# Performance work log

Hardware: AMD Instinct MI355X
Metric: run time of the kernel (lower is better)

Reference implementation:

```python
import jax, jax.numpy as jnp
import numpy as np

DIM = 256
HEADS = 8
WIN = 8
N = WIN * WIN          # 64 tokens per window
NW = 1024              # windows per image (256x256 map, 8x8 windows)
BATCH = 4
B_ = BATCH * NW        # 4096
HEAD_DIM = DIM // HEADS


def _relative_position_index():
    # identical to the torch buffer construction in WindowAttention.__init__
    coords = np.stack(np.meshgrid(np.arange(WIN), np.arange(WIN), indexing='ij'))  # [2,W,W]
    flat = coords.reshape(2, -1)                                # [2, N]
    rel = flat[:, :, None] - flat[:, None, :]                   # [2, N, N]
    rel = rel.transpose(1, 2, 0).copy()                         # [N, N, 2]
    rel[:, :, 0] += WIN - 1
    rel[:, :, 1] += WIN - 1
    rel[:, :, 0] *= 2 * WIN - 1
    return jnp.asarray(rel.sum(-1), dtype=jnp.int32)            # [N, N], values in [0, 225)


def setup_inputs() -> dict:
    key = jax.random.key(0)
    ks = jax.random.split(key, 9)
    std = 0.02
    return {
        'x': jax.random.normal(ks[0], (B_, N, DIM), dtype=jnp.float32),
        'mask': jax.random.normal(ks[1], (NW, N, N), dtype=jnp.float32),
        'w_q': jax.random.normal(ks[2], (DIM, DIM), dtype=jnp.float32) * std,
        'b_q': jnp.zeros((DIM,), dtype=jnp.float32),
        'w_kv': jax.random.normal(ks[3], (2 * DIM, DIM), dtype=jnp.float32) * std,
        'b_kv': jnp.zeros((2 * DIM,), dtype=jnp.float32),
        'bias_table': jax.random.normal(ks[4], ((2 * WIN - 1) ** 2, HEADS), dtype=jnp.float32) * std,
        'w_o': jax.random.normal(ks[5], (DIM, DIM), dtype=jnp.float32) * std,
        'b_o': jnp.zeros((DIM,), dtype=jnp.float32),
        'rp_index': _relative_position_index(),
    }


def reference(x, mask, w_q, b_q, w_kv, b_kv, bias_table, w_o, b_o, rp_index):
    Bw, n, c = x.shape
    h, d = HEADS, c // HEADS
    scale = d ** -0.5

    # linear QKV projection (LinearProjection with attn_kv=None)
    q = (x @ w_q.T + b_q).reshape(Bw, n, h, d).transpose(0, 2, 1, 3)      # [B_, H, N, D]
    kv = (x @ w_kv.T + b_kv).reshape(Bw, n, 2, h, d).transpose(2, 0, 3, 1, 4)
    k, v = kv[0], kv[1]                                                    # [B_, H, N, D]

    # scaled QK^T
    attn = jnp.einsum('bhnd,bhmd->bhnm', q * scale, k)                     # [B_, H, N, N]

    # gathered relative position bias (ratio = 1 since attn_kv is None)
    bias = bias_table[rp_index]                                            # [N, N, H]
    attn = attn + bias.transpose(2, 0, 1)[None]                            # broadcast over B_

    # per-window additive mask
    nW = mask.shape[0]
    attn = attn.reshape(Bw // nW, nW, h, n, n) + mask[None, :, None]
    attn = attn.reshape(Bw, h, n, n)

    attn = jax.nn.softmax(attn, axis=-1)

    out = jnp.einsum('bhnm,bhmd->bhnd', attn, v)                           # [B_, H, N, D]
    out = out.transpose(0, 2, 1, 3).reshape(Bw, n, c)
    return out @ w_o.T + b_o
```

## Files before the change

### kernel.cpp

```cpp
#include <hip/hip_runtime.h>
#include <hip/hip_bf16.h>

typedef __bf16 bf16_t;
typedef bf16_t bf16x8 __attribute__((ext_vector_type(8)));
typedef bf16_t bf16x4 __attribute__((ext_vector_type(4)));
typedef float f32x4 __attribute__((ext_vector_type(4)));

#define WS_WKV_OFF 65536
#define WS_WO_OFF  196608
#define WS_B8_OFF  524288

__global__ __launch_bounds__(256) void prep_kernel(
    const float* __restrict__ wq, const float* __restrict__ wkv,
    const float* __restrict__ wo, const float* __restrict__ bt,
    const int* __restrict__ rp,
    bf16_t* __restrict__ wsq, bf16_t* __restrict__ wskv,
    bf16_t* __restrict__ wso, float* __restrict__ bias8) {
  int t = blockIdx.x * 256 + threadIdx.x;
  if (t < 65536)  wsq[t]  = (bf16_t)wq[t];
  if (t < 131072) wskv[t] = (bf16_t)wkv[t];
  if (t < 65536)  wso[t]  = (bf16_t)wo[t];
  if (t < 4096) {
    int idx = rp[t];
#pragma unroll
    for (int h = 0; h < 8; ++h) bias8[h * 4096 + t] = bt[idx * 8 + h];
  }
}

#define LDS_TOTAL_BYTES 152576

__global__ __launch_bounds__(512, 2) void win_attn_kernel(
    const float* __restrict__ x, const float* __restrict__ mask,
    const float* __restrict__ bq, const float* __restrict__ bkv,
    const float* __restrict__ bo,
    const bf16_t* __restrict__ wsq, const bf16_t* __restrict__ wskv,
    const bf16_t* __restrict__ wso, const float* __restrict__ bias8,
    float* __restrict__ out) {
  extern __shared__ bf16_t lds[];
  const int b    = blockIdx.x;
  const int tid  = threadIdx.x;
  const int wid  = tid >> 6;
  const int lane = tid & 63;
  const int lrow = lane & 15;
  const int lgrp = lane >> 4;

  {
    const float4* xv = (const float4*)(x + (size_t)b * 16384);
#pragma unroll
    for (int j = 0; j < 8; ++j) {
      int i4 = j * 512 + tid;
      float4 v = xv[i4];
      int e = i4 * 4;
      int r = e >> 8, c = e & 255;
      bf16x4 w = {(bf16_t)v.x, (bf16_t)v.y, (bf16_t)v.z, (bf16_t)v.w};
      *(bf16x4*)(lds + r * 264 + c) = w;
    }
  }
  __syncthreads();

  const int h = wid;
  bf16_t* ldsQ  = lds + 16896 + wid * 7424;
  bf16_t* ldsK  = ldsQ + 2560;
  bf16_t* ldsVt = ldsQ + 5120;
  bf16_t* ldsP  = ldsQ;
  bf16_t* ldsO  = lds;

  const bf16_t* WQh = wsq  + h * 32 * 256;
  const bf16_t* WKh = wskv + h * 32 * 256;
  const bf16_t* WVh = wskv + (256 + h * 32) * 256;
  f32x4 aq[4][2], ak[4][2], av[4][2];
  const f32x4 zf = {0.f, 0.f, 0.f, 0.f};
#pragma unroll
  for (int tm = 0; tm < 4; ++tm)
#pragma unroll
    for (int tn = 0; tn < 2; ++tn) { aq[tm][tn] = zf; ak[tm][tn] = zf; av[tm][tn] = zf; }

#pragma unroll
  for (int ks = 0; ks < 8; ++ks) {
    bf16x8 af[4];
#pragma unroll
    for (int tm = 0; tm < 4; ++tm)
      af[tm] = *(const bf16x8*)(lds + (tm * 16 + lrow) * 264 + ks * 32 + lgrp * 8);
    bf16x8 bqf[2], bkf[2], bvf[2];
#pragma unroll
    for (int tn = 0; tn < 2; ++tn) {
      int wr = (tn * 16 + lrow) * 256 + ks * 32 + lgrp * 8;
      bqf[tn] = *(const bf16x8*)(WQh + wr);
      bkf[tn] = *(const bf16x8*)(WKh + wr);
      bvf[tn] = *(const bf16x8*)(WVh + wr);
    }
#pragma unroll
    for (int tm = 0; tm < 4; ++tm)
#pragma unroll
      for (int tn = 0; tn < 2; ++tn) {
        aq[tm][tn] = __builtin_amdgcn_mfma_f32_16x16x32_bf16(af[tm], bqf[tn], aq[tm][tn], 0, 0, 0);
        ak[tm][tn] = __builtin_amdgcn_mfma_f32_16x16x32_bf16(af[tm], bkf[tn], ak[tm][tn], 0, 0, 0);
        av[tm][tn] = __builtin_amdgcn_mfma_f32_16x16x32_bf16(af[tm], bvf[tn], av[tm][tn], 0, 0, 0);
      }
  }

  const float scale = 0.17677669529663687f;
#pragma unroll
  for (int tn = 0; tn < 2; ++tn) {
    float bqv = bq[h * 32 + tn * 16 + lrow];
    float bkv_ = bkv[h * 32 + tn * 16 + lrow];
    float bvv = bkv[256 + h * 32 + tn * 16 + lrow];
#pragma unroll
    for (int tm = 0; tm < 4; ++tm) {
#pragma unroll
      for (int r = 0; r < 4; ++r) {
        int row = tm * 16 + lgrp * 4 + r;
        ldsQ[row * 40 + tn * 16 + lrow] = (bf16_t)((aq[tm][tn][r] + bqv) * scale);
        ldsK[row * 40 + tn * 16 + lrow] = (bf16_t)(ak[tm][tn][r] + bkv_);
      }
      bf16x4 vv;
#pragma unroll
      for (int r = 0; r < 4; ++r) vv[r] = (bf16_t)(av[tm][tn][r] + bvv);
      *(bf16x4*)(ldsVt + (tn * 16 + lrow) * 72 + tm * 16 + lgrp * 4) = vv;
    }
  }
  __syncthreads();

  f32x4 s[4][4];
  {
    bf16x8 qf[4], kf[4];
#pragma unroll
    for (int t = 0; t < 4; ++t) {
      qf[t] = *(const bf16x8*)(ldsQ + (t * 16 + lrow) * 40 + lgrp * 8);
      kf[t] = *(const bf16x8*)(ldsK + (t * 16 + lrow) * 40 + lgrp * 8);
    }
#pragma unroll
    for (int tm = 0; tm < 4; ++tm)
#pragma unroll
      for (int tc = 0; tc < 4; ++tc)
        s[tm][tc] = __builtin_amdgcn_mfma_f32_16x16x32_bf16(qf[tm], kf[tc], zf, 0, 0, 0);
  }
  const float* maskw = mask + (size_t)(b & 1023) * 4096;
  const float* biash = bias8 + h * 4096;
  float rs[4][4];
#pragma unroll
  for (int tm = 0; tm < 4; ++tm) {
    float val[4][4];
    float mx[4] = {-1e30f, -1e30f, -1e30f, -1e30f};
#pragma unroll
    for (int tc = 0; tc < 4; ++tc)
#pragma unroll
      for (int r = 0; r < 4; ++r) {
        int row = tm * 16 + lgrp * 4 + r, col = tc * 16 + lrow;
        float v = s[tm][tc][r] + biash[row * 64 + col] + maskw[row * 64 + col];
        val[tc][r] = v;
        mx[r] = fmaxf(mx[r], v);
      }
#pragma unroll
    for (int r = 0; r < 4; ++r) {
      float m = mx[r];
      m = fmaxf(m, __shfl_xor(m, 1));
      m = fmaxf(m, __shfl_xor(m, 2));
      m = fmaxf(m, __shfl_xor(m, 4));
      m = fmaxf(m, __shfl_xor(m, 8));
      mx[r] = m;
    }
    float sm[4] = {0.f, 0.f, 0.f, 0.f};
#pragma unroll
    for (int tc = 0; tc < 4; ++tc)
#pragma unroll
      for (int r = 0; r < 4; ++r) {
        float p = __expf(val[tc][r] - mx[r]);
        val[tc][r] = p;
        sm[r] += p;
      }
#pragma unroll
    for (int r = 0; r < 4; ++r) {
      float t = sm[r];
      t += __shfl_xor(t, 1);
      t += __shfl_xor(t, 2);
      t += __shfl_xor(t, 4);
      t += __shfl_xor(t, 8);
      rs[tm][r] = 1.0f / t;
    }
#pragma unroll
    for (int tc = 0; tc < 4; ++tc)
#pragma unroll
      for (int r = 0; r < 4; ++r)
        ldsP[(tm * 16 + lgrp * 4 + r) * 72 + tc * 16 + lrow] = (bf16_t)val[tc][r];
  }

  f32x4 o[4][2];
#pragma unroll
  for (int tm = 0; tm < 4; ++tm)
#pragma unroll
    for (int tn = 0; tn < 2; ++tn) o[tm][tn] = zf;
#pragma unroll
  for (int ks = 0; ks < 2; ++ks) {
    bf16x8 pf[4], vf[2];
#pragma unroll
    for (int tm = 0; tm < 4; ++tm)
      pf[tm] = *(const bf16x8*)(ldsP + (tm * 16 + lrow) * 72 + ks * 32 + lgrp * 8);
#pragma unroll
    for (int tn = 0; tn < 2; ++tn)
      vf[tn] = *(const bf16x8*)(ldsVt + (tn * 16 + lrow) * 72 + ks * 32 + lgrp * 8);
#pragma unroll
    for (int tm = 0; tm < 4; ++tm)
#pragma unroll
      for (int tn = 0; tn < 2; ++tn)
        o[tm][tn] = __builtin_amdgcn_mfma_f32_16x16x32_bf16(pf[tm], vf[tn], o[tm][tn], 0, 0, 0);
  }
#pragma unroll
  for (int tm = 0; tm < 4; ++tm)
#pragma unroll
    for (int tn = 0; tn < 2; ++tn)
#pragma unroll
      for (int r = 0; r < 4; ++r)
        ldsO[(tm * 16 + lgrp * 4 + r) * 264 + h * 32 + tn * 16 + lrow] =
            (bf16_t)(o[tm][tn][r] * rs[tm][r]);
  __syncthreads();

  const int nb = wid * 32;
  f32x4 oc[4][2];
#pragma unroll
  for (int tm = 0; tm < 4; ++tm)
#pragma unroll
    for (int tn = 0; tn < 2; ++tn) oc[tm][tn] = zf;
#pragma unroll
  for (int ks = 0; ks < 8; ++ks) {
    bf16x8 af[4], bf_[2];
#pragma unroll
    for (int tm = 0; tm < 4; ++tm)
      af[tm] = *(const bf16x8*)(ldsO + (tm * 16 + lrow) * 264 + ks * 32 + lgrp * 8);
#pragma unroll
    for (int tn = 0; tn < 2; ++tn)
      bf_[tn] = *(const bf16x8*)(wso + (nb + tn * 16 + lrow) * 256 + ks * 32 + lgrp * 8);
#pragma unroll
    for (int tm = 0; tm < 4; ++tm)
#pragma unroll
      for (int tn = 0; tn < 2; ++tn)
        oc[tm][tn] = __builtin_amdgcn_mfma_f32_16x16x32_bf16(af[tm], bf_[tn], oc[tm][tn], 0, 0, 0);
  }
  float* outw = out + (size_t)b * 16384;
#pragma unroll
  for (int tn = 0; tn < 2; ++tn) {
    float bov = bo[nb + tn * 16 + lrow];
#pragma unroll
    for (int tm = 0; tm < 4; ++tm)
#pragma unroll
      for (int r = 0; r < 4; ++r)
        outw[(tm * 16 + lgrp * 4 + r) * 256 + nb + tn * 16 + lrow] = oc[tm][tn][r] + bov;
  }
}

extern "C" void kernel_launch(void* const* d_in, const int* in_sizes, int n_in,
                              void* d_out, int out_size, void* d_ws, size_t ws_size,
                              hipStream_t stream) {
  const float* x    = (const float*)d_in[0];
  const float* mask = (const float*)d_in[1];
  const float* wq   = (const float*)d_in[2];
  const float* bq   = (const float*)d_in[3];
  const float* wkv  = (const float*)d_in[4];
  const float* bkv  = (const float*)d_in[5];
  const float* bt   = (const float*)d_in[6];
  const float* wo   = (const float*)d_in[7];
  const float* bo   = (const float*)d_in[8];
  const int*   rp   = (const int*)d_in[9];
  float* out = (float*)d_out;

  bf16_t* wsq  = (bf16_t*)d_ws;
  bf16_t* wskv = wsq + WS_WKV_OFF;
  bf16_t* wso  = wsq + WS_WO_OFF;
  float*  bias8 = (float*)((char*)d_ws + WS_B8_OFF);

  prep_kernel<<<512, 256, 0, stream>>>(wq, wkv, wo, bt, rp, wsq, wskv, wso, bias8);

  (void)hipFuncSetAttribute((const void*)win_attn_kernel,
                            hipFuncAttributeMaxDynamicSharedMemorySize, LDS_TOTAL_BYTES);
  win_attn_kernel<<<4096, 512, LDS_TOTAL_BYTES, stream>>>(
      x, mask, bq, bkv, bo, wsq, wskv, wso, bias8, out);
}
```

Measured before the change: 608.1 us.

## Split each window across 16 waves by row slab and stage output through LDS

Block size doubles to 1024 threads. Each head is now handled by two waves, each owning a 32-row slab of the 64 tokens, which halves per-wave MFMA work and register accumulators. The final projection result is staged in LDS and written to global memory with coalesced float4 stores instead of strided scalar stores. This adds extra barriers, and the QKV projection now loads each weight fragment twice per block. The launch bound of 1024 threads with 4 blocks requested may force register pressure or spills, while LDS still limits residency to one block per CU.

```diff
diff --git a/kernel.cpp b/kernel.cpp
--- a/kernel.cpp
+++ b/kernel.cpp
@@ -29,7 +29,7 @@
 
 #define LDS_TOTAL_BYTES 152576
 
-__global__ __launch_bounds__(512, 2) void win_attn_kernel(
+__global__ __launch_bounds__(1024, 4) void win_attn_kernel(
     const float* __restrict__ x, const float* __restrict__ mask,
     const float* __restrict__ bq, const float* __restrict__ bkv,
     const float* __restrict__ bo,
@@ -43,12 +43,15 @@
   const int lane = tid & 63;
   const int lrow = lane & 15;
   const int lgrp = lane >> 4;
+  const int h    = wid & 7;
+  const int slab = wid >> 3;
+  const int r0   = slab * 32;
 
   {
     const float4* xv = (const float4*)(x + (size_t)b * 16384);
 #pragma unroll
-    for (int j = 0; j < 8; ++j) {
-      int i4 = j * 512 + tid;
+    for (int j = 0; j < 4; ++j) {
+      int i4 = j * 1024 + tid;
       float4 v = xv[i4];
       int e = i4 * 4;
       int r = e >> 8, c = e & 255;
@@ -58,29 +61,29 @@
   }
   __syncthreads();
 
-  const int h = wid;
-  bf16_t* ldsQ  = lds + 16896 + wid * 7424;
+  bf16_t* ldsQ  = lds + 16896 + h * 7424;
   bf16_t* ldsK  = ldsQ + 2560;
   bf16_t* ldsVt = ldsQ + 5120;
   bf16_t* ldsP  = ldsQ;
   bf16_t* ldsO  = lds;
+  float*  stage = (float*)(lds + 16896);
 
   const bf16_t* WQh = wsq  + h * 32 * 256;
   const bf16_t* WKh = wskv + h * 32 * 256;
   const bf16_t* WVh = wskv + (256 + h * 32) * 256;
-  f32x4 aq[4][2], ak[4][2], av[4][2];
+  f32x4 aq[2][2], ak[2][2], av[2][2];
   const f32x4 zf = {0.f, 0.f, 0.f, 0.f};
 #pragma unroll
-  for (int tm = 0; tm < 4; ++tm)
+  for (int tm = 0; tm < 2; ++tm)
 #pragma unroll
     for (int tn = 0; tn < 2; ++tn) { aq[tm][tn] = zf; ak[tm][tn] = zf; av[tm][tn] = zf; }
 
 #pragma unroll
   for (int ks = 0; ks < 8; ++ks) {
-    bf16x8 af[4];
-#pragma unroll
-    for (int tm = 0; tm < 4; ++tm)
-      af[tm] = *(const bf16x8*)(lds + (tm * 16 + lrow) * 264 + ks * 32 + lgrp * 8);
+    bf16x8 af[2];
+#pragma unroll
+    for (int tm = 0; tm < 2; ++tm)
+      af[tm] = *(const bf16x8*)(lds + (r0 + tm * 16 + lrow) * 264 + ks * 32 + lgrp * 8);
     bf16x8 bqf[2], bkf[2], bvf[2];
 #pragma unroll
     for (int tn = 0; tn < 2; ++tn) {
@@ -90,7 +93,7 @@
       bvf[tn] = *(const bf16x8*)(WVh + wr);
     }
 #pragma unroll
-    for (int tm = 0; tm < 4; ++tm)
+    for (int tm = 0; tm < 2; ++tm)
 #pragma unroll
       for (int tn = 0; tn < 2; ++tn) {
         aq[tm][tn] = __builtin_amdgcn_mfma_f32_16x16x32_bf16(af[tm], bqf[tn], aq[tm][tn], 0, 0, 0);
@@ -102,51 +105,54 @@
   const float scale = 0.17677669529663687f;
 #pragma unroll
   for (int tn = 0; tn < 2; ++tn) {
-    float bqv = bq[h * 32 + tn * 16 + lrow];
+    float bqv  = bq[h * 32 + tn * 16 + lrow];
     float bkv_ = bkv[h * 32 + tn * 16 + lrow];
-    float bvv = bkv[256 + h * 32 + tn * 16 + lrow];
-#pragma unroll
-    for (int tm = 0; tm < 4; ++tm) {
+    float bvv  = bkv[256 + h * 32 + tn * 16 + lrow];
+#pragma unroll
+    for (int tm = 0; tm < 2; ++tm) {
 #pragma unroll
       for (int r = 0; r < 4; ++r) {
-        int row = tm * 16 + lgrp * 4 + r;
+        int row = r0 + tm * 16 + lgrp * 4 + r;
         ldsQ[row * 40 + tn * 16 + lrow] = (bf16_t)((aq[tm][tn][r] + bqv) * scale);
         ldsK[row * 40 + tn * 16 + lrow] = (bf16_t)(ak[tm][tn][r] + bkv_);
       }
       bf16x4 vv;
 #pragma unroll
       for (int r = 0; r < 4; ++r) vv[r] = (bf16_t)(av[tm][tn][r] + bvv);
-      *(bf16x4*)(ldsVt + (tn * 16 + lrow) * 72 + tm * 16 + lgrp * 4) = vv;
-    }
-  }
-  __syncthreads();
-
-  f32x4 s[4][4];
+      *(bf16x4*)(ldsVt + (tn * 16 + lrow) * 72 + r0 + tm * 16 + lgrp * 4) = vv;
+    }
+  }
+  __syncthreads();
+
+  f32x4 s[2][4];
   {
-    bf16x8 qf[4], kf[4];
-#pragma unroll
-    for (int t = 0; t < 4; ++t) {
-      qf[t] = *(const bf16x8*)(ldsQ + (t * 16 + lrow) * 40 + lgrp * 8);
+    bf16x8 qf[2], kf[4];
+#pragma unroll
+    for (int t = 0; t < 2; ++t)
+      qf[t] = *(const bf16x8*)(ldsQ + (r0 + t * 16 + lrow) * 40 + lgrp * 8);
+#pragma unroll
+    for (int t = 0; t < 4; ++t)
       kf[t] = *(const bf16x8*)(ldsK + (t * 16 + lrow) * 40 + lgrp * 8);
-    }
-#pragma unroll
-    for (int tm = 0; tm < 4; ++tm)
+#pragma unroll
+    for (int tm = 0; tm < 2; ++tm)
 #pragma unroll
       for (int tc = 0; tc < 4; ++tc)
         s[tm][tc] = __builtin_amdgcn_mfma_f32_16x16x32_bf16(qf[tm], kf[tc], zf, 0, 0, 0);
   }
+  __syncthreads();
+
   const float* maskw = mask + (size_t)(b & 1023) * 4096;
   const float* biash = bias8 + h * 4096;
-  float rs[4][4];
-#pragma unroll
-  for (int tm = 0; tm < 4; ++tm) {
+  float rs[2][4];
+#pragma unroll
+  for (int tm = 0; tm < 2; ++tm) {
     float val[4][4];
     float mx[4] = {-1e30f, -1e30f, -1e30f, -1e30f};
 #pragma unroll
     for (int tc = 0; tc < 4; ++tc)
 #pragma unroll
       for (int r = 0; r < 4; ++r) {
-        int row = tm * 16 + lgrp * 4 + r, col = tc * 16 + lrow;
+        int row = r0 + tm * 16 + lgrp * 4 + r, col = tc * 16 + lrow;
         float v = s[tm][tc][r] + biash[row * 64 + col] + maskw[row * 64 + col];
         val[tc][r] = v;
         mx[r] = fmaxf(mx[r], v);
@@ -182,69 +188,81 @@
     for (int tc = 0; tc < 4; ++tc)
 #pragma unroll
       for (int r = 0; r < 4; ++r)
-        ldsP[(tm * 16 + lgrp * 4 + r) * 72 + tc * 16 + lrow] = (bf16_t)val[tc][r];
-  }
-
-  f32x4 o[4][2];
-#pragma unroll
-  for (int tm = 0; tm < 4; ++tm)
+        ldsP[(r0 + tm * 16 + lgrp * 4 + r) * 72 + tc * 16 + lrow] = (bf16_t)val[tc][r];
+  }
+
+  f32x4 o[2][2];
+#pragma unroll
+  for (int tm = 0; tm < 2; ++tm)
 #pragma unroll
     for (int tn = 0; tn < 2; ++tn) o[tm][tn] = zf;
 #pragma unroll
   for (int ks = 0; ks < 2; ++ks) {
-    bf16x8 pf[4], vf[2];
-#pragma unroll
-    for (int tm = 0; tm < 4; ++tm)
-      pf[tm] = *(const bf16x8*)(ldsP + (tm * 16 + lrow) * 72 + ks * 32 + lgrp * 8);
+    bf16x8 pf[2], vf[2];
+#pragma unroll
+    for (int tm = 0; tm < 2; ++tm)
+      pf[tm] = *(const bf16x8*)(ldsP + (r0 + tm * 16 + lrow) * 72 + ks * 32 + lgrp * 8);
 #pragma unroll
     for (int tn = 0; tn < 2; ++tn)
       vf[tn] = *(const bf16x8*)(ldsVt + (tn * 16 + lrow) * 72 + ks * 32 + lgrp * 8);
 #pragma unroll
-    for (int tm = 0; tm < 4; ++tm)
+    for (int tm = 0; tm < 2; ++tm)
 #pragma unroll
       for (int tn = 0; tn < 2; ++tn)
         o[tm][tn] = __builtin_amdgcn_mfma_f32_16x16x32_bf16(pf[tm], vf[tn], o[tm][tn], 0, 0, 0);
   }
 #pragma unroll
-  for (int tm = 0; tm < 4; ++tm)
+  for (int tm = 0; tm < 2; ++tm)
 #pragma unroll
     for (int tn = 0; tn < 2; ++tn)
 #pragma unroll
       for (int r = 0; r < 4; ++r)
-        ldsO[(tm * 16 + lgrp * 4 + r) * 264 + h * 32 + tn * 16 + lrow] =
+        ldsO[(r0 + tm * 16 + lgrp * 4 + r) * 264 + h * 32 + tn * 16 + lrow] =
             (bf16_t)(o[tm][tn][r] * rs[tm][r]);
   __syncthreads();
 
-  const int nb = wid * 32;
-  f32x4 oc[4][2];
-#pragma unroll
-  for (int tm = 0; tm < 4; ++tm)
+  const int nb = h * 32;
+  f32x4 oc[2][2];
+#pragma unroll
+  for (int tm = 0; tm < 2; ++tm)
 #pragma unroll
     for (int tn = 0; tn < 2; ++tn) oc[tm][tn] = zf;
 #pragma unroll
   for (int ks = 0; ks < 8; ++ks) {
-    bf16x8 af[4], bf_[2];
-#pragma unroll
-    for (int tm = 0; tm < 4; ++tm)
-      af[tm] = *(const bf16x8*)(ldsO + (tm * 16 + lrow) * 264 + ks * 32 + lgrp * 8);
+    bf16x8 af[2], bf_[2];
+#pragma unroll
+    for (int tm = 0; tm < 2; ++tm)
+      af[tm] = *(const bf16x8*)(ldsO + (r0 + tm * 16 + lrow) * 264 + ks * 32 + lgrp * 8);
 #pragma unroll
     for (int tn = 0; tn < 2; ++tn)
       bf_[tn] = *(const bf16x8*)(wso + (nb + tn * 16 + lrow) * 256 + ks * 32 + lgrp * 8);
 #pragma unroll
-    for (int tm = 0; tm < 4; ++tm)
+    for (int tm = 0; tm < 2; ++tm)
 #pragma unroll
       for (int tn = 0; tn < 2; ++tn)
         oc[tm][tn] = __builtin_amdgcn_mfma_f32_16x16x32_bf16(af[tm], bf_[tn], oc[tm][tn], 0, 0, 0);
   }
-  float* outw = out + (size_t)b * 16384;
 #pragma unroll
   for (int tn = 0; tn < 2; ++tn) {
     float bov = bo[nb + tn * 16 + lrow];
 #pragma unroll
-    for (int tm = 0; tm < 4; ++tm)
+    for (int tm = 0; tm < 2; ++tm)
 #pragma unroll
       for (int r = 0; r < 4; ++r)
-        outw[(tm * 16 + lgrp * 4 + r) * 256 + nb + tn * 16 + lrow] = oc[tm][tn][r] + bov;
+        stage[(r0 + tm * 16 + lgrp * 4 + r) * 260 + nb + tn * 16 + lrow] =
+            oc[tm][tn][r] + bov;
+  }
+  __syncthreads();
+
+  {
+    float* outw = out + (size_t)b * 16384;
+#pragma unroll
+    for (int j = 0; j < 4; ++j) {
+      int idx = j * 1024 + tid;
+      int r = idx >> 6, c = (idx & 63) * 4;
+      float4 v = *(const float4*)(stage + r * 260 + c);
+      *(float4*)(outw + r * 256 + c) = v;
+    }
   }
 }
 
@@ -272,6 +290,6 @@
 
   (void)hipFuncSetAttribute((const void*)win_attn_kernel,
                             hipFuncAttributeMaxDynamicSharedMemorySize, LDS_TOTAL_BYTES);
-  win_attn_kernel<<<4096, 512, LDS_TOTAL_BYTES, stream>>>(
+  win_attn_kernel<<<4096, 1024, LDS_TOTAL_BYTES, stream>>>(
       x, mask, bq, bkv, bo, wsq, wskv, wso, bias8, out);
 }
```

After: 655.4 us. +7.8%, slower.

## Keep Q/K/V/P in registers via bpermute transposes, shrink LDS for higher occupancy

Applied to the files above, without the earlier changes.

Per-head Q, K, V and softmax probabilities now stay in registers, and MFMA fragments are rearranged with ds_bpermute lane shuffles instead of being staged through per-wave LDS buffers. LDS drops to a single 64x264 bf16 tile, and launch bounds move from 2 to 4 blocks per CU. The Q scale is folded into the bf16 weights in the prep kernel, and scores are computed transposed so mask and bias load as float4. The cost is higher register pressure and extra permute instructions, which may cause spills under the tighter launch bounds.

```diff
diff --git a/kernel.cpp b/kernel.cpp
--- a/kernel.cpp
+++ b/kernel.cpp
@@ -1,14 +1,18 @@
 #include <hip/hip_runtime.h>
 #include <hip/hip_bf16.h>
+#include <stdint.h>
 
 typedef __bf16 bf16_t;
 typedef bf16_t bf16x8 __attribute__((ext_vector_type(8)));
 typedef bf16_t bf16x4 __attribute__((ext_vector_type(4)));
+typedef bf16_t bf16x2 __attribute__((ext_vector_type(2)));
 typedef float f32x4 __attribute__((ext_vector_type(4)));
+typedef uint32_t u32x4 __attribute__((ext_vector_type(4)));
 
 #define WS_WKV_OFF 65536
 #define WS_WO_OFF  196608
 #define WS_B8_OFF  524288
+#define QSCALE 0.17677669529663687f
 
 __global__ __launch_bounds__(256) void prep_kernel(
     const float* __restrict__ wq, const float* __restrict__ wkv,
@@ -17,7 +21,7 @@
     bf16_t* __restrict__ wsq, bf16_t* __restrict__ wskv,
     bf16_t* __restrict__ wso, float* __restrict__ bias8) {
   int t = blockIdx.x * 256 + threadIdx.x;
-  if (t < 65536)  wsq[t]  = (bf16_t)wq[t];
+  if (t < 65536)  wsq[t]  = (bf16_t)(wq[t] * QSCALE);
   if (t < 131072) wskv[t] = (bf16_t)wkv[t];
   if (t < 65536)  wso[t]  = (bf16_t)wo[t];
   if (t < 4096) {
@@ -27,22 +31,48 @@
   }
 }
 
-#define LDS_TOTAL_BYTES 152576
-
-__global__ __launch_bounds__(512, 2) void win_attn_kernel(
+__device__ __forceinline__ bf16x8 xpose_frag(uint32_t e0, uint32_t e1,
+                                             uint32_t o0, uint32_t o1,
+                                             int ad0, int ad1, bool hi) {
+  uint32_t v0e = (uint32_t)__builtin_amdgcn_ds_bpermute(ad0, (int)e0);
+  uint32_t v0o = (uint32_t)__builtin_amdgcn_ds_bpermute(ad0, (int)o0);
+  uint32_t v1e = (uint32_t)__builtin_amdgcn_ds_bpermute(ad0, (int)e1);
+  uint32_t v1o = (uint32_t)__builtin_amdgcn_ds_bpermute(ad0, (int)o1);
+  uint32_t v2e = (uint32_t)__builtin_amdgcn_ds_bpermute(ad1, (int)e0);
+  uint32_t v2o = (uint32_t)__builtin_amdgcn_ds_bpermute(ad1, (int)o0);
+  uint32_t v3e = (uint32_t)__builtin_amdgcn_ds_bpermute(ad1, (int)e1);
+  uint32_t v3o = (uint32_t)__builtin_amdgcn_ds_bpermute(ad1, (int)o1);
+  u32x4 r;
+  r.x = hi ? v0o : v0e;
+  r.y = hi ? v1o : v1e;
+  r.z = hi ? v2o : v2e;
+  r.w = hi ? v3o : v3e;
+  return __builtin_bit_cast(bf16x8, r);
+}
+
+__device__ __forceinline__ uint32_t pk2(float a, float b) {
+  bf16x2 t = {(bf16_t)a, (bf16_t)b};
+  return __builtin_bit_cast(uint32_t, t);
+}
+
+__global__ __launch_bounds__(512, 4) void win_attn_kernel(
     const float* __restrict__ x, const float* __restrict__ mask,
     const float* __restrict__ bq, const float* __restrict__ bkv,
     const float* __restrict__ bo,
     const bf16_t* __restrict__ wsq, const bf16_t* __restrict__ wskv,
     const bf16_t* __restrict__ wso, const float* __restrict__ bias8,
     float* __restrict__ out) {
-  extern __shared__ bf16_t lds[];
+  __shared__ bf16_t lds[64 * 264];
   const int b    = blockIdx.x;
   const int tid  = threadIdx.x;
-  const int wid  = tid >> 6;
+  const int h    = tid >> 6;
   const int lane = tid & 63;
   const int lrow = lane & 15;
   const int lgrp = lane >> 4;
+  const bool hi  = (lgrp & 2) != 0;
+  const int ad0  = ((((2 * lgrp) & 3) << 4) + lrow) << 2;
+  const int ad1  = ((((2 * lgrp + 1) & 3) << 4) + lrow) << 2;
+  const f32x4 zf = {0.f, 0.f, 0.f, 0.f};
 
   {
     const float4* xv = (const float4*)(x + (size_t)b * 16384);
@@ -58,183 +88,190 @@
   }
   __syncthreads();
 
-  const int h = wid;
-  bf16_t* ldsQ  = lds + 16896 + wid * 7424;
-  bf16_t* ldsK  = ldsQ + 2560;
-  bf16_t* ldsVt = ldsQ + 5120;
-  bf16_t* ldsP  = ldsQ;
-  bf16_t* ldsO  = lds;
-
   const bf16_t* WQh = wsq  + h * 32 * 256;
   const bf16_t* WKh = wskv + h * 32 * 256;
-  const bf16_t* WVh = wskv + (256 + h * 32) * 256;
-  f32x4 aq[4][2], ak[4][2], av[4][2];
-  const f32x4 zf = {0.f, 0.f, 0.f, 0.f};
-#pragma unroll
-  for (int tm = 0; tm < 4; ++tm)
-#pragma unroll
-    for (int tn = 0; tn < 2; ++tn) { aq[tm][tn] = zf; ak[tm][tn] = zf; av[tm][tn] = zf; }
-
+  f32x4 aq[2][4], akk[2][4];
+#pragma unroll
+  for (int tm = 0; tm < 2; ++tm)
+#pragma unroll
+    for (int tn = 0; tn < 4; ++tn) { aq[tm][tn] = zf; akk[tm][tn] = zf; }
 #pragma unroll
   for (int ks = 0; ks < 8; ++ks) {
-    bf16x8 af[4];
-#pragma unroll
-    for (int tm = 0; tm < 4; ++tm)
-      af[tm] = *(const bf16x8*)(lds + (tm * 16 + lrow) * 264 + ks * 32 + lgrp * 8);
-    bf16x8 bqf[2], bkf[2], bvf[2];
-#pragma unroll
-    for (int tn = 0; tn < 2; ++tn) {
-      int wr = (tn * 16 + lrow) * 256 + ks * 32 + lgrp * 8;
-      bqf[tn] = *(const bf16x8*)(WQh + wr);
-      bkf[tn] = *(const bf16x8*)(WKh + wr);
-      bvf[tn] = *(const bf16x8*)(WVh + wr);
-    }
+    bf16x8 xb[4];
+#pragma unroll
+    for (int tn = 0; tn < 4; ++tn)
+      xb[tn] = *(const bf16x8*)(lds + (tn * 16 + lrow) * 264 + ks * 32 + lgrp * 8);
+    bf16x8 wqf[2], wkf[2];
+#pragma unroll
+    for (int tm = 0; tm < 2; ++tm) {
+      int off = (tm * 16 + lrow) * 256 + ks * 32 + lgrp * 8;
+      wqf[tm] = *(const bf16x8*)(WQh + off);
+      wkf[tm] = *(const bf16x8*)(WKh + off);
+    }
+#pragma unroll
+    for (int tm = 0; tm < 2; ++tm)
+#pragma unroll
+      for (int tn = 0; tn < 4; ++tn) {
+        aq[tm][tn]  = __builtin_amdgcn_mfma_f32_16x16x32_bf16(wqf[tm], xb[tn], aq[tm][tn], 0, 0, 0);
+        akk[tm][tn] = __builtin_amdgcn_mfma_f32_16x16x32_bf16(wkf[tm], xb[tn], akk[tm][tn], 0, 0, 0);
+      }
+  }
+  bf16x8 qb[4], ka[4];
+  {
+    uint32_t pkq[2][4][2], pkk[2][4][2];
+#pragma unroll
+    for (int tm = 0; tm < 2; ++tm) {
+      float4 b4 = *(const float4*)(bq + h * 32 + tm * 16 + lgrp * 4);
+      float4 k4 = *(const float4*)(bkv + h * 32 + tm * 16 + lgrp * 4);
+      float bqa[4] = {b4.x * QSCALE, b4.y * QSCALE, b4.z * QSCALE, b4.w * QSCALE};
+      float bka[4] = {k4.x, k4.y, k4.z, k4.w};
+#pragma unroll
+      for (int tn = 0; tn < 4; ++tn)
+#pragma unroll
+        for (int pr = 0; pr < 2; ++pr) {
+          pkq[tm][tn][pr] = pk2(aq[tm][tn][2 * pr] + bqa[2 * pr],
+                                aq[tm][tn][2 * pr + 1] + bqa[2 * pr + 1]);
+          pkk[tm][tn][pr] = pk2(akk[tm][tn][2 * pr] + bka[2 * pr],
+                                akk[tm][tn][2 * pr + 1] + bka[2 * pr + 1]);
+        }
+    }
+#pragma unroll
+    for (int t = 0; t < 4; ++t) {
+      qb[t] = xpose_frag(pkq[0][t][0], pkq[0][t][1], pkq[1][t][0], pkq[1][t][1], ad0, ad1, hi);
+      ka[t] = xpose_frag(pkk[0][t][0], pkk[0][t][1], pkk[1][t][0], pkk[1][t][1], ad0, ad1, hi);
+    }
+  }
+
+  bf16x8 vb[2][2];
+  {
+    const bf16_t* WVh = wskv + (256 + h * 32) * 256;
+    f32x4 av[4][2];
+#pragma unroll
+    for (int tm = 0; tm < 4; ++tm)
+#pragma unroll
+      for (int tn = 0; tn < 2; ++tn) av[tm][tn] = zf;
+#pragma unroll
+    for (int ks = 0; ks < 8; ++ks) {
+      bf16x8 xa[4];
+#pragma unroll
+      for (int tm = 0; tm < 4; ++tm)
+        xa[tm] = *(const bf16x8*)(lds + (tm * 16 + lrow) * 264 + ks * 32 + lgrp * 8);
+      bf16x8 wvf[2];
+#pragma unroll
+      for (int tn = 0; tn < 2; ++tn)
+        wvf[tn] = *(const bf16x8*)(WVh + (tn * 16 + lrow) * 256 + ks * 32 + lgrp * 8);
+#pragma unroll
+      for (int tm = 0; tm < 4; ++tm)
+#pragma unroll
+        for (int tn = 0; tn < 2; ++tn)
+          av[tm][tn] = __builtin_amdgcn_mfma_f32_16x16x32_bf16(xa[tm], wvf[tn], av[tm][tn], 0, 0, 0);
+    }
+    float bv0 = bkv[256 + h * 32 + lrow];
+    float bv1 = bkv[256 + h * 32 + 16 + lrow];
+    uint32_t pkv[4][2][2];
 #pragma unroll
     for (int tm = 0; tm < 4; ++tm)
 #pragma unroll
       for (int tn = 0; tn < 2; ++tn) {
-        aq[tm][tn] = __builtin_amdgcn_mfma_f32_16x16x32_bf16(af[tm], bqf[tn], aq[tm][tn], 0, 0, 0);
-        ak[tm][tn] = __builtin_amdgcn_mfma_f32_16x16x32_bf16(af[tm], bkf[tn], ak[tm][tn], 0, 0, 0);
-        av[tm][tn] = __builtin_amdgcn_mfma_f32_16x16x32_bf16(af[tm], bvf[tn], av[tm][tn], 0, 0, 0);
+        float bv = tn ? bv1 : bv0;
+#pragma unroll
+        for (int pr = 0; pr < 2; ++pr)
+          pkv[tm][tn][pr] = pk2(av[tm][tn][2 * pr] + bv, av[tm][tn][2 * pr + 1] + bv);
       }
-  }
-
-  const float scale = 0.17677669529663687f;
-#pragma unroll
-  for (int tn = 0; tn < 2; ++tn) {
-    float bqv = bq[h * 32 + tn * 16 + lrow];
-    float bkv_ = bkv[h * 32 + tn * 16 + lrow];
-    float bvv = bkv[256 + h * 32 + tn * 16 + lrow];
-#pragma unroll
-    for (int tm = 0; tm < 4; ++tm) {
-#pragma unroll
-      for (int r = 0; r < 4; ++r) {
-        int row = tm * 16 + lgrp * 4 + r;
-        ldsQ[row * 40 + tn * 16 + lrow] = (bf16_t)((aq[tm][tn][r] + bqv) * scale);
-        ldsK[row * 40 + tn * 16 + lrow] = (bf16_t)(ak[tm][tn][r] + bkv_);
-      }
-      bf16x4 vv;
-#pragma unroll
-      for (int r = 0; r < 4; ++r) vv[r] = (bf16_t)(av[tm][tn][r] + bvv);
-      *(bf16x4*)(ldsVt + (tn * 16 + lrow) * 72 + tm * 16 + lgrp * 4) = vv;
-    }
-  }
+#pragma unroll
+    for (int dt = 0; dt < 2; ++dt)
+#pragma unroll
+      for (int kf = 0; kf < 2; ++kf)
+        vb[dt][kf] = xpose_frag(pkv[2 * kf][dt][0], pkv[2 * kf][dt][1],
+                                pkv[2 * kf + 1][dt][0], pkv[2 * kf + 1][dt][1], ad0, ad1, hi);
+  }
+
   __syncthreads();
 
-  f32x4 s[4][4];
-  {
-    bf16x8 qf[4], kf[4];
-#pragma unroll
-    for (int t = 0; t < 4; ++t) {
-      qf[t] = *(const bf16x8*)(ldsQ + (t * 16 + lrow) * 40 + lgrp * 8);
-      kf[t] = *(const bf16x8*)(ldsK + (t * 16 + lrow) * 40 + lgrp * 8);
-    }
-#pragma unroll
-    for (int tm = 0; tm < 4; ++tm)
-#pragma unroll
-      for (int tc = 0; tc < 4; ++tc)
-        s[tm][tc] = __builtin_amdgcn_mfma_f32_16x16x32_bf16(qf[tm], kf[tc], zf, 0, 0, 0);
-  }
   const float* maskw = mask + (size_t)(b & 1023) * 4096;
   const float* biash = bias8 + h * 4096;
-  float rs[4][4];
-#pragma unroll
-  for (int tm = 0; tm < 4; ++tm) {
-    float val[4][4];
-    float mx[4] = {-1e30f, -1e30f, -1e30f, -1e30f};
-#pragma unroll
-    for (int tc = 0; tc < 4; ++tc)
+#pragma unroll
+  for (int qt = 0; qt < 4; ++qt) {
+    f32x4 st[4];
+#pragma unroll
+    for (int tm = 0; tm < 4; ++tm)
+      st[tm] = __builtin_amdgcn_mfma_f32_16x16x32_bf16(ka[tm], qb[qt], zf, 0, 0, 0);
+    int q = qt * 16 + lrow;
+#pragma unroll
+    for (int tm = 0; tm < 4; ++tm) {
+      int kb = tm * 16 + lgrp * 4;
+      float4 mb = *(const float4*)(maskw + q * 64 + kb);
+      float4 bb = *(const float4*)(biash + q * 64 + kb);
+      st[tm][0] += mb.x + bb.x;
+      st[tm][1] += mb.y + bb.y;
+      st[tm][2] += mb.z + bb.z;
+      st[tm][3] += mb.w + bb.w;
+    }
+    float mx = -1e30f;
+#pragma unroll
+    for (int tm = 0; tm < 4; ++tm)
+#pragma unroll
+      for (int r = 0; r < 4; ++r) mx = fmaxf(mx, st[tm][r]);
+    mx = fmaxf(mx, __shfl_xor(mx, 16));
+    mx = fmaxf(mx, __shfl_xor(mx, 32));
+    float sm = 0.f;
+#pragma unroll
+    for (int tm = 0; tm < 4; ++tm)
 #pragma unroll
       for (int r = 0; r < 4; ++r) {
-        int row = tm * 16 + lgrp * 4 + r, col = tc * 16 + lrow;
-        float v = s[tm][tc][r] + biash[row * 64 + col] + maskw[row * 64 + col];
-        val[tc][r] = v;
-        mx[r] = fmaxf(mx[r], v);
+        float p = __expf(st[tm][r] - mx);
+        st[tm][r] = p;
+        sm += p;
       }
-#pragma unroll
-    for (int r = 0; r < 4; ++r) {
-      float m = mx[r];
-      m = fmaxf(m, __shfl_xor(m, 1));
-      m = fmaxf(m, __shfl_xor(m, 2));
-      m = fmaxf(m, __shfl_xor(m, 4));
-      m = fmaxf(m, __shfl_xor(m, 8));
-      mx[r] = m;
-    }
-    float sm[4] = {0.f, 0.f, 0.f, 0.f};
-#pragma unroll
-    for (int tc = 0; tc < 4; ++tc)
-#pragma unroll
-      for (int r = 0; r < 4; ++r) {
-        float p = __expf(val[tc][r] - mx[r]);
-        val[tc][r] = p;
-        sm[r] += p;
-      }
-#pragma unroll
-    for (int r = 0; r < 4; ++r) {
-      float t = sm[r];
-      t += __shfl_xor(t, 1);
-      t += __shfl_xor(t, 2);
-      t += __shfl_xor(t, 4);
-      t += __shfl_xor(t, 8);
-      rs[tm][r] = 1.0f / t;
-    }
-#pragma unroll
-    for (int tc = 0; tc < 4; ++tc)
+    sm += __shfl_xor(sm, 16);
+    sm += __shfl_xor(sm, 32);
+    float rs = 1.0f / sm;
+    uint32_t ppk[4][2];
+#pragma unroll
+    for (int tm = 0; tm < 4; ++tm) {
+      ppk[tm][0] = pk2(st[tm][0] * rs, st[tm][1] * rs);
+      ppk[tm][1] = pk2(st[tm][2] * rs, st[tm][3] * rs);
+    }
+    bf16x8 paf[2];
+#pragma unroll
+    for (int kf = 0; kf < 2; ++kf)
+      paf[kf] = xpose_frag(ppk[2 * kf][0], ppk[2 * kf][1],
+                           ppk[2 * kf + 1][0], ppk[2 * kf + 1][1], ad0, ad1, hi);
+    f32x4 o[2] = {zf, zf};
+#pragma unroll
+    for (int dt = 0; dt < 2; ++dt) {
+      o[dt] = __builtin_amdgcn_mfma_f32_16x16x32_bf16(paf[0], vb[dt][0], o[dt], 0, 0, 0);
+      o[dt] = __builtin_amdgcn_mfma_f32_16x16x32_bf16(paf[1], vb[dt][1], o[dt], 0, 0, 0);
+    }
+#pragma unroll
+    for (int dt = 0; dt < 2; ++dt)
 #pragma unroll
       for (int r = 0; r < 4; ++r)
-        ldsP[(tm * 16 + lgrp * 4 + r) * 72 + tc * 16 + lrow] = (bf16_t)val[tc][r];
-  }
-
-  f32x4 o[4][2];
+        lds[(qt * 16 + lgrp * 4 + r) * 264 + h * 32 + dt * 16 + lrow] = (bf16_t)o[dt][r];
+  }
+  __syncthreads();
+
+  const int nb = h * 32;
+  f32x4 oc[4][2];
 #pragma unroll
   for (int tm = 0; tm < 4; ++tm)
 #pragma unroll
-    for (int tn = 0; tn < 2; ++tn) o[tm][tn] = zf;
-#pragma unroll
-  for (int ks = 0; ks < 2; ++ks) {
-    bf16x8 pf[4], vf[2];
-#pragma unroll
-    for (int tm = 0; tm < 4; ++tm)
-      pf[tm] = *(const bf16x8*)(ldsP + (tm * 16 + lrow) * 72 + ks * 32 + lgrp * 8);
+    for (int tn = 0; tn < 2; ++tn) oc[tm][tn] = zf;
+#pragma unroll
+  for (int ks = 0; ks < 8; ++ks) {
+    bf16x8 ao[4];
+#pragma unroll
+    for (int tm = 0; tm < 4; ++tm)
+      ao[tm] = *(const bf16x8*)(lds + (tm * 16 + lrow) * 264 + ks * 32 + lgrp * 8);
+    bf16x8 bw[2];
 #pragma unroll
     for (int tn = 0; tn < 2; ++tn)
-      vf[tn] = *(const bf16x8*)(ldsVt + (tn * 16 + lrow) * 72 + ks * 32 + lgrp * 8);
+      bw[tn] = *(const bf16x8*)(wso + (nb + tn * 16 + lrow) * 256 + ks * 32 + lgrp * 8);
 #pragma unroll
     for (int tm = 0; tm < 4; ++tm)
 #pragma unroll
       for (int tn = 0; tn < 2; ++tn)
-        o[tm][tn] = __builtin_amdgcn_mfma_f32_16x16x32_bf16(pf[tm], vf[tn], o[tm][tn], 0, 0, 0);
-  }
-#pragma unroll
-  for (int tm = 0; tm < 4; ++tm)
-#pragma unroll
-    for (int tn = 0; tn < 2; ++tn)
-#pragma unroll
-      for (int r = 0; r < 4; ++r)
-        ldsO[(tm * 16 + lgrp * 4 + r) * 264 + h * 32 + tn * 16 + lrow] =
-            (bf16_t)(o[tm][tn][r] * rs[tm][r]);
-  __syncthreads();
-
-  const int nb = wid * 32;
-  f32x4 oc[4][2];
-#pragma unroll
-  for (int tm = 0; tm < 4; ++tm)
-#pragma unroll
-    for (int tn = 0; tn < 2; ++tn) oc[tm][tn] = zf;
-#pragma unroll
-  for (int ks = 0; ks < 8; ++ks) {
-    bf16x8 af[4], bf_[2];
-#pragma unroll
-    for (int tm = 0; tm < 4; ++tm)
-      af[tm] = *(const bf16x8*)(ldsO + (tm * 16 + lrow) * 264 + ks * 32 + lgrp * 8);
-#pragma unroll
-    for (int tn = 0; tn < 2; ++tn)
-      bf_[tn] = *(const bf16x8*)(wso + (nb + tn * 16 + lrow) * 256 + ks * 32 + lgrp * 8);
-#pragma unroll
-    for (int tm = 0; tm < 4; ++tm)
-#pragma unroll
-      for (int tn = 0; tn < 2; ++tn)
-        oc[tm][tn] = __builtin_amdgcn_mfma_f32_16x16x32_bf16(af[tm], bf_[tn], oc[tm][tn], 0, 0, 0);
+        oc[tm][tn] = __builtin_amdgcn_mfma_f32_16x16x32_bf16(ao[tm], bw[tn], oc[tm][tn], 0, 0, 0);
   }
   float* outw = out + (size_t)b * 16384;
 #pragma unroll
@@ -270,8 +307,6 @@
 
   prep_kernel<<<512, 256, 0, stream>>>(wq, wkv, wo, bt, rp, wsq, wskv, wso, bias8);
 
-  (void)hipFuncSetAttribute((const void*)win_attn_kernel,
-                            hipFuncAttributeMaxDynamicSharedMemorySize, LDS_TOTAL_BYTES);
-  win_attn_kernel<<<4096, 512, LDS_TOTAL_BYTES, stream>>>(
+  win_attn_kernel<<<4096, 512, 0, stream>>>(
       x, mask, bq, bkv, bo, wsq, wskv, wso, bias8, out);
 }
```

New measurement: 932.1 us. +53.3%, slower.
